# Kernel tuning notes

Measured on AMD Instinct MI355X. Metric: run time of the kernel, lower is better.

Reference implementation:

```python
import jax, jax.numpy as jnp
import numpy as np

N_CHANNELS = 1024
N_HEADS = 16
SEQ = 2048
BATCH = 2


def setup_inputs() -> dict:
    key = jax.random.key(0)
    k1, k2, k3 = jax.random.split(key, 3)
    x = jax.random.normal(k1, (BATCH, SEQ, N_CHANNELS), dtype=jnp.float32)
    qkv_w = jax.random.normal(k2, (3 * N_CHANNELS, N_CHANNELS), dtype=jnp.float32) * 0.02
    qkv_b = jnp.zeros((3 * N_CHANNELS,), dtype=jnp.float32)
    proj_w = jax.random.normal(k3, (N_CHANNELS, N_CHANNELS), dtype=jnp.float32) * 0.02
    proj_b = jnp.zeros((N_CHANNELS,), dtype=jnp.float32)
    return {"x": x, "qkv_w": qkv_w, "qkv_b": qkv_b, "proj_w": proj_w, "proj_b": proj_b}


def reference(x, qkv_w, qkv_b, proj_w, proj_b):
    bs, t, c = x.shape
    h = N_HEADS
    hd = c // h
    scale = hd ** (-0.5)
    # qkv projection: torch Linear is x @ W^T + b
    qkv = x @ qkv_w.T + qkv_b  # [B, T, 3C]
    qkv = qkv.reshape(bs, t, 3, h, hd)
    q, k, v = qkv[:, :, 0], qkv[:, :, 1], qkv[:, :, 2]  # each [B, T, H, hd]
    logits = jnp.einsum('bthc,bshc->bhts', q, k) * scale  # [B, H, T, T]
    # causal mask: log(tril(ones)) -> 0 below diag, -inf above
    causal = jnp.tril(jnp.ones((t, t), dtype=bool))
    logits = jnp.where(causal[None, None], logits, -jnp.inf)
    attn = jax.nn.softmax(logits, axis=-1)
    out = jnp.einsum('bhts,bshc->bthc', attn, v).reshape(bs, t, c)
    out = out @ proj_w.T + proj_b
    return out
```

## Files before the change

### kernel.cpp

```cpp
#include <hip/hip_runtime.h>

typedef __bf16 bf16x8 __attribute__((ext_vector_type(8)));
typedef float f32x4 __attribute__((ext_vector_type(4)));
typedef float f32x16 __attribute__((ext_vector_type(16)));

__device__ inline ushort f2bf(float f) {
    unsigned u = __builtin_bit_cast(unsigned, f);
    unsigned r = (u + 0x7FFFu + ((u >> 16) & 1u)) >> 16;
    return (ushort)r;
}
__device__ inline float bf2f(ushort u) {
    unsigned x = ((unsigned)u) << 16;
    return __builtin_bit_cast(float, x);
}
__device__ inline uint4 pack8(const float* f) {
    uint4 r;
    r.x = (unsigned)f2bf(f[0]) | ((unsigned)f2bf(f[1]) << 16);
    r.y = (unsigned)f2bf(f[2]) | ((unsigned)f2bf(f[3]) << 16);
    r.z = (unsigned)f2bf(f[4]) | ((unsigned)f2bf(f[5]) << 16);
    r.w = (unsigned)f2bf(f[6]) | ((unsigned)f2bf(f[7]) << 16);
    return r;
}
__device__ inline unsigned cvtpk_bf16(float lo, float hi) {
    unsigned r;
    asm("v_cvt_pk_bf16_f32 %0, %1, %2" : "=v"(r) : "v"(lo), "v"(hi));
    return r;
}

#define MFMA_BF16(a, b, c) __builtin_amdgcn_mfma_f32_16x16x32_bf16(a, b, c, 0, 0, 0)
#define MFMA32(a, b, c) __builtin_amdgcn_mfma_f32_32x32x16_bf16(a, b, c, 0, 0, 0)
#define GLDS(g, l) __builtin_amdgcn_global_load_lds( \
    (const __attribute__((address_space(1))) void*)(g), \
    (__attribute__((address_space(3))) void*)(l), 16, 0, 0)

#define QSCALE 0.18033688011112042f

__global__ __launch_bounds__(256) void convert3(
    const float* __restrict__ s0, ushort* __restrict__ d0,
    const float* __restrict__ s1, ushort* __restrict__ d1,
    const float* __restrict__ s2, ushort* __restrict__ d2)
{
    const int i = blockIdx.x * 256 + threadIdx.x;
    const float* s; ushort* d; int off;
    if (i < 524288)      { s = s0; d = d0; off = i; }
    else if (i < 917504) { s = s1; d = d1; off = i - 524288; }
    else                 { s = s2; d = d2; off = i - 917504; }
    const float4* f = (const float4*)s + off * 2;
    float fa[8];
    *(float4*)&fa[0] = f[0];
    *(float4*)&fa[4] = f[1];
    ((uint4*)d)[off] = pack8(fa);
}

__global__ __launch_bounds__(256) void gemm_qkv(
    const ushort* __restrict__ A, const ushort* __restrict__ B,
    const float* __restrict__ bias,
    ushort* __restrict__ outQ, ushort* __restrict__ outK, ushort* __restrict__ outV,
    int N, int K)
{
    __shared__ __align__(16) ushort SMEM[32768];

    const int tid = threadIdx.x;
    const int w = tid >> 6;
    const int lane = tid & 63;
    const int l15 = lane & 15;
    const int quad = lane >> 4;
    const int srow = lane >> 3;

    const int bid = blockIdx.x + (blockIdx.y << 5);
    const int nb = (bid & 7) * 96 + (bid >> 3);
    const int m0 = (nb / 24) * 128;
    const int n0 = (nb % 24) * 128;
    const int wr = (w & 1) * 64;
    const int wc = (w >> 1) * 64;

    auto stage = [&](int k0, int buf) {
        ushort* As = SMEM + buf * 16384;
        ushort* Bs = As + 8192;
#pragma unroll
        for (int j = 0; j < 4; j++) {
            const int r0 = w * 32 + j * 8;
            const int row = r0 + srow;
            const int gcol = ((lane & 7) ^ (row & 7)) * 8;
            GLDS(A + (size_t)(m0 + row) * K + k0 + gcol, As + r0 * 64);
            GLDS(B + (size_t)(n0 + row) * K + k0 + gcol, Bs + r0 * 64);
        }
    };

    f32x4 acc[4][4] = {};

    stage(0, 0);
    __syncthreads();

    for (int k0 = 0; k0 < K; k0 += 64) {
        const int cur = (k0 >> 6) & 1;
        if (k0 + 64 < K) stage(k0 + 64, cur ^ 1);

        const ushort* As = SMEM + cur * 16384;
        const ushort* Bs = As + 8192;
        bf16x8 af[4][2], bf[4][2];
#pragma unroll
        for (int i = 0; i < 4; i++)
#pragma unroll
            for (int kk = 0; kk < 2; kk++) {
                const int ra = wr + i * 16 + l15;
                const int rb = wc + i * 16 + l15;
                af[i][kk] = *(const bf16x8*)&As[ra * 64 + (((kk * 4 + quad) ^ (ra & 7)) * 8)];
                bf[i][kk] = *(const bf16x8*)&Bs[rb * 64 + (((kk * 4 + quad) ^ (rb & 7)) * 8)];
            }
#pragma unroll
        for (int kk = 0; kk < 2; kk++)
#pragma unroll
            for (int mi = 0; mi < 4; mi++)
#pragma unroll
                for (int ni = 0; ni < 4; ni++)
                    acc[mi][ni] = MFMA_BF16(af[mi][kk], bf[ni][kk], acc[mi][ni]);
        __syncthreads();
    }

    const int which = n0 >> 10;
    ushort* Ct = SMEM;
    if (which == 2) {
#pragma unroll
        for (int mi = 0; mi < 4; mi++)
#pragma unroll
            for (int ni = 0; ni < 4; ni++)
#pragma unroll
                for (int r = 0; r < 4; r++) {
                    const int m_loc = wr + mi * 16 + quad * 4 + r;
                    const int n_loc = wc + ni * 16 + l15;
                    Ct[n_loc * 136 + m_loc] =
                        f2bf(acc[mi][ni][r] + bias[n0 + n_loc]);
                }
        __syncthreads();
        const int b = m0 >> 11;
#pragma unroll
        for (int i = 0; i < 8; i++) {
            const int vi = tid + i * 256;
            const int n_loc = vi >> 4, mblk = vi & 15;
            const uint4 val = *(const uint4*)&Ct[n_loc * 136 + mblk * 8];
            const int t = (m0 & 2047) + mblk * 8;
            const int c = (n0 + n_loc) & 1023;
            const int h = c >> 6, d = c & 63;
            *(uint4*)&outV[((size_t)(b * 16 + h) * 64 + d) * 2048 + t] = val;
        }
    } else {
        const float qs = (which == 0) ? QSCALE : 1.0f;
#pragma unroll
        for (int mi = 0; mi < 4; mi++)
#pragma unroll
            for (int ni = 0; ni < 4; ni++)
#pragma unroll
                for (int r = 0; r < 4; r++) {
                    const int m_loc = wr + mi * 16 + quad * 4 + r;
                    const int n_loc = wc + ni * 16 + l15;
                    Ct[m_loc * 136 + n_loc] =
                        f2bf((acc[mi][ni][r] + bias[n0 + n_loc]) * qs);
                }
        __syncthreads();
        ushort* outP = (which == 0) ? outQ : outK;
        const int hb = (n0 & 1023) >> 6;
        const int b = m0 >> 11;
#pragma unroll
        for (int i = 0; i < 8; i++) {
            const int vi = tid + i * 256;
            const int m_loc = vi >> 4, u = vi & 15;
            const uint4 val = *(const uint4*)&Ct[m_loc * 136 + u * 8];
            const int t = (m0 & 2047) + m_loc;
            const int h = hb + (u >> 3);
            const int d8 = (u & 7) * 8;
            *(uint4*)&outP[((size_t)(b * 16 + h)) * 131072 + (size_t)t * 64 + d8] = val;
        }
    }
}

__global__ __launch_bounds__(256) void gemm_proj(
    const ushort* __restrict__ A, const ushort* __restrict__ B,
    const float* __restrict__ bias, float* __restrict__ outD)
{
    const int N = 1024, K = 1024;
    __shared__ __align__(16) ushort SMEM[24576];

    const int tid = threadIdx.x;
    const int w = tid >> 6;
    const int lane = tid & 63;
    const int l15 = lane & 15;
    const int quad = lane >> 4;
    const int srow = lane >> 3;

    const int bid = blockIdx.x + (blockIdx.y << 6);
    const int nb = (bid & 7) * 64 + (bid >> 3);
    const int m0 = (nb >> 3) * 64;
    const int n0 = (nb & 7) * 128;
    const int wr = (w & 1) * 32;
    const int wc = (w >> 1) * 64;

    auto stage = [&](int k0, int buf) {
        ushort* As = SMEM + buf * 12288;
        ushort* Bs = As + 4096;
#pragma unroll
        for (int j = 0; j < 2; j++) {
            const int r0 = w * 16 + j * 8;
            const int row = r0 + srow;
            const int gcol = ((lane & 7) ^ (row & 7)) * 8;
            GLDS(A + (size_t)(m0 + row) * K + k0 + gcol, As + r0 * 64);
        }
#pragma unroll
        for (int j = 0; j < 4; j++) {
            const int r0 = w * 32 + j * 8;
            const int row = r0 + srow;
            const int gcol = ((lane & 7) ^ (row & 7)) * 8;
            GLDS(B + (size_t)(n0 + row) * K + k0 + gcol, Bs + r0 * 64);
        }
    };

    f32x4 acc[2][4] = {};

    stage(0, 0);
    __syncthreads();

    for (int k0 = 0; k0 < K; k0 += 64) {
        const int cur = (k0 >> 6) & 1;
        if (k0 + 64 < K) stage(k0 + 64, cur ^ 1);

        const ushort* As = SMEM + cur * 12288;
        const ushort* Bs = As + 4096;
        bf16x8 af[2][2], bf[4][2];
#pragma unroll
        for (int kk = 0; kk < 2; kk++) {
#pragma unroll
            for (int mi = 0; mi < 2; mi++) {
                const int ra = wr + mi * 16 + l15;
                af[mi][kk] = *(const bf16x8*)&As[ra * 64 + (((kk * 4 + quad) ^ (ra & 7)) * 8)];
            }
#pragma unroll
            for (int ni = 0; ni < 4; ni++) {
                const int rb = wc + ni * 16 + l15;
                bf[ni][kk] = *(const bf16x8*)&Bs[rb * 64 + (((kk * 4 + quad) ^ (rb & 7)) * 8)];
            }
        }
#pragma unroll
        for (int kk = 0; kk < 2; kk++)
#pragma unroll
            for (int mi = 0; mi < 2; mi++)
#pragma unroll
                for (int ni = 0; ni < 4; ni++)
                    acc[mi][ni] = MFMA_BF16(af[mi][kk], bf[ni][kk], acc[mi][ni]);
        __syncthreads();
    }

    float* Cf = (float*)SMEM;
#pragma unroll
    for (int cch = 0; cch < 2; cch++) {
        __syncthreads();
        if ((wc >> 6) == cch) {
#pragma unroll
            for (int mi = 0; mi < 2; mi++)
#pragma unroll
                for (int ni = 0; ni < 4; ni++)
#pragma unroll
                    for (int r = 0; r < 4; r++) {
                        const int m_loc = wr + mi * 16 + quad * 4 + r;
                        const int nl = ni * 16 + l15;
                        Cf[m_loc * 68 + nl] = acc[mi][ni][r] + bias[n0 + cch * 64 + nl];
                    }
        }
        __syncthreads();
#pragma unroll
        for (int i = 0; i < 4; i++) {
            const int vi = tid + i * 256;
            const int m_loc = vi >> 4, u = vi & 15;
            const float4 val = *(const float4*)&Cf[m_loc * 68 + u * 4];
            *(float4*)&outD[(size_t)(m0 + m_loc) * N + n0 + cch * 64 + u * 4] = val;
        }
    }
}

__global__ __launch_bounds__(256, 4) void attn_split(
    const ushort* __restrict__ Q, const ushort* __restrict__ K,
    const ushort* __restrict__ Vt, ushort* __restrict__ O,
    ushort* __restrict__ Opart, float* __restrict__ Lpart)
{
    __shared__ __align__(16) ushort KV[2][2][64 * 64];

    const int bh = blockIdx.x;
    const int y = blockIdx.y;
    int qt, k0, k1, chunk, split;
    if (y < 24) {
        qt = 15 - (y >> 1); chunk = y & 1; split = 1;
        const int h2 = qt + 1;
        k0 = chunk ? h2 : 0; k1 = chunk ? 2 * qt + 2 : h2;
    } else {
        qt = 27 - y; chunk = 0; split = 0; k0 = 0; k1 = 2 * qt + 2;
    }
    const int q0 = qt * 128;
    const int tid = threadIdx.x;
    const int w = tid >> 6;
    const int lane = tid & 63;
    const int l31 = lane & 31;
    const int hf = lane >> 5;
    const int wrow0 = q0 + w * 32;
    const int rowg = wrow0 + l31;

    auto stage = [&](int kt, int b) {
        const int t0 = kt * 64;
#pragma unroll
        for (int j = 0; j < 2; j++) {
            const int r0 = w * 16 + j * 8;
            const int row = r0 + (lane >> 3);
            const int gcol = ((lane & 7) ^ (row & 7)) * 8;
            GLDS(K + ((size_t)bh * 2048 + t0 + row) * 64 + gcol, &KV[b][0][r0 * 64]);
            GLDS(Vt + ((size_t)bh * 64 + row) * 2048 + t0 + gcol, &KV[b][1][r0 * 64]);
        }
    };

    const ushort* qbase = Q + ((size_t)bh * 2048 + rowg) * 64 + hf * 8;
    bf16x8 qf[4];
#pragma unroll
    for (int db = 0; db < 4; db++) qf[db] = *(const bf16x8*)(qbase + db * 16);

    bf16x8 ones;
#pragma unroll
    for (int j = 0; j < 8; j++) ones[j] = (__bf16)1.0f;

    f32x16 oacc[2] = {};
    f32x16 lacc = {};

    stage(k0, 0);

    for (int kt = k0; kt < k1; kt++) {
        __syncthreads();
        if (kt + 1 < k1) stage(kt + 1, (kt + 1 - k0) & 1);

        const ushort* Ks = &KV[(kt - k0) & 1][0][0];
        const ushort* Vs = &KV[(kt - k0) & 1][1][0];
        const int t0 = kt * 64;

        if (t0 <= wrow0 + 31) {
            f32x16 sacc[2] = {};
#pragma unroll
            for (int db = 0; db < 4; db++)
#pragma unroll
                for (int kb = 0; kb < 2; kb++) {
                    const int rr = kb * 32 + l31;
                    bf16x8 kf = *(const bf16x8*)&Ks[rr * 64 + (((db * 2 + hf) ^ (rr & 7)) * 8)];
                    sacc[kb] = MFMA32(kf, qf[db], sacc[kb]);
                }

            unsigned u[2][8];
            const bool nm = (t0 + 63 > wrow0);
#pragma unroll
            for (int kb = 0; kb < 2; kb++) {
                float p[16];
                if (nm) {
#pragma unroll
                    for (int reg = 0; reg < 16; reg++) {
                        const int col = t0 + kb * 32 + (reg & 3) + 8 * (reg >> 2) + 4 * hf;
                        float x = (col > rowg) ? -1e30f : sacc[kb][reg];
                        p[reg] = __builtin_exp2f(x);
                    }
                } else {
#pragma unroll
                    for (int reg = 0; reg < 16; reg++)
                        p[reg] = __builtin_exp2f(sacc[kb][reg]);
                }
#pragma unroll
                for (int t = 0; t < 8; t++)
                    u[kb][t] = cvtpk_bf16(p[2 * t], p[2 * t + 1]);
            }

#pragma unroll
            for (int kb = 0; kb < 2; kb++)
#pragma unroll
                for (int g = 0; g < 4; g++) {
                    const int tp = (g & 1) + (g >> 1) * 4;
                    asm("v_permlane32_swap_b32 %0, %1"
                        : "+v"(u[kb][tp]), "+v"(u[kb][tp + 2]));
                }

#pragma unroll
            for (int m = 0; m < 4; m++) {
                uint4 av;
                av.x = u[m >> 1][(m & 1) * 4 + 0];
                av.y = u[m >> 1][(m & 1) * 4 + 1];
                av.z = u[m >> 1][(m & 1) * 4 + 2];
                av.w = u[m >> 1][(m & 1) * 4 + 3];
                bf16x8 af = __builtin_bit_cast(bf16x8, av);
                lacc = MFMA32(af, ones, lacc);
#pragma unroll
                for (int d2 = 0; d2 < 2; d2++) {
                    const int rr = d2 * 32 + l31;
                    bf16x8 vf = *(const bf16x8*)&Vs[rr * 64 + (((m * 2 + hf) ^ (rr & 7)) * 8)];
                    oacc[d2] = MFMA32(af, vf, oacc[d2]);
                }
            }
        }
    }

    if (!split) {
        const int b = bh >> 4, hh = bh & 15;
#pragma unroll
        for (int reg = 0; reg < 16; reg++) {
            const int rowf = (reg & 3) + 8 * (reg >> 2) + 4 * hf;
            const float inv = 1.0f / lacc[reg];
            const int row = wrow0 + rowf;
#pragma unroll
            for (int d2 = 0; d2 < 2; d2++)
                O[((size_t)b * 2048 + row) * 1024 + hh * 64 + d2 * 32 + l31] =
                    f2bf(oacc[d2][reg] * inv);
        }
    } else {
        const size_t slot2 = ((size_t)bh * 12 + (qt - 4)) * 2 + chunk;
        if (l31 == 0) {
#pragma unroll
            for (int reg = 0; reg < 16; reg++)
                Lpart[slot2 * 128 + w * 32 + (reg & 3) + 8 * (reg >> 2) + 4 * hf] = lacc[reg];
        }
#pragma unroll
        for (int reg = 0; reg < 16; reg++) {
            const int rl = w * 32 + (reg & 3) + 8 * (reg >> 2) + 4 * hf;
#pragma unroll
            for (int d2 = 0; d2 < 2; d2++)
                Opart[slot2 * 8192 + rl * 64 + d2 * 32 + l31] = f2bf(oacc[d2][reg]);
        }
    }
}

__global__ __launch_bounds__(256) void attn_combine(
    const ushort* __restrict__ Opart, const float* __restrict__ Lpart,
    ushort* __restrict__ O)
{
    const int bh = blockIdx.x;
    const int qt = 4 + blockIdx.y;
    const int tid = threadIdx.x;
    const int row = tid >> 1;
    const int dg = (tid & 1) * 32;
    const size_t s = ((size_t)bh * 12 + (qt - 4)) * 2;
    const ushort* p0 = Opart + s * 8192 + row * 64 + dg;
    const ushort* p1 = p0 + 8192;
    const float inv = 1.0f / (Lpart[s * 128 + row] + Lpart[(s + 1) * 128 + row]);
    const int b = bh >> 4, hh = bh & 15;
    ushort* dst = O + ((size_t)b * 2048 + qt * 128 + row) * 1024 + hh * 64 + dg;
#pragma unroll
    for (int v = 0; v < 4; v++) {
        uint4 a = *(const uint4*)(p0 + v * 8);
        uint4 c = *(const uint4*)(p1 + v * 8);
        const ushort* ua = (const ushort*)&a;
        const ushort* uc = (const ushort*)&c;
        ushort out[8];
#pragma unroll
        for (int j = 0; j < 8; j++)
            out[j] = f2bf((bf2f(ua[j]) + bf2f(uc[j])) * inv);
        *(uint4*)(dst + v * 8) = *(uint4*)out;
    }
}

extern "C" void kernel_launch(void* const* d_in, const int* in_sizes, int n_in,
                              void* d_out, int out_size, void* d_ws, size_t ws_size,
                              hipStream_t stream) {
    const float* x      = (const float*)d_in[0];
    const float* qkv_w  = (const float*)d_in[1];
    const float* qkv_b  = (const float*)d_in[2];
    const float* proj_w = (const float*)d_in[3];
    const float* proj_b = (const float*)d_in[4];

    ushort* XbOb  = (ushort*)d_ws + 16;
    ushort* Wqkv  = XbOb + 4194304;
    ushort* Wproj = Wqkv + 3145728;
    ushort* Qb    = Wproj + 1048576;
    ushort* Kb    = Qb + 4194304;
    ushort* Vt    = Kb + 4194304;
    ushort* Opart = Vt + 4194304;
    float*  Lpart = (float*)(Opart + 6291456);

    convert3<<<4096, 256, 0, stream>>>(x, XbOb, qkv_w, Wqkv, proj_w, Wproj);
    gemm_qkv<<<dim3(32, 24), 256, 0, stream>>>(XbOb, Wqkv, qkv_b,
                                               Qb, Kb, Vt, 3072, 1024);
    attn_split<<<dim3(32, 28), 256, 0, stream>>>(Qb, Kb, Vt, XbOb, Opart, Lpart);
    attn_combine<<<dim3(32, 12), 256, 0, stream>>>(Opart, Lpart, XbOb);
    gemm_proj<<<dim3(64, 8), 256, 0, stream>>>(XbOb, Wproj, proj_b, (float*)d_out);
}
```

Baseline: 209.1 us.

## Rebalance causal attention split with 2/3/4-way KV chunks and staged coalesced output

Longer causal query tiles are now split into 2, 3 or 4 KV chunks according to their length instead of always 2, raising the grid from 28 to 40 tiles per head so per-block work is more even. Block IDs are remapped so that neighbouring IDs land on different XCDs, output tiles are staged through shared memory for coalesced 16-byte stores, and the occupancy hint rises to 5. The combine kernel now sums a variable number of partials, and the Opart buffer reuses the Wqkv workspace region. The cost is more partial-result traffic and combine work, plus an added barrier in each block.

```diff
diff --git a/kernel.cpp b/kernel.cpp
--- a/kernel.cpp
+++ b/kernel.cpp
@@ -276,22 +276,32 @@
     }
 }
 
-__global__ __launch_bounds__(256, 4) void attn_split(
+__global__ __launch_bounds__(256, 5) void attn_split(
     const ushort* __restrict__ Q, const ushort* __restrict__ K,
     const ushort* __restrict__ Vt, ushort* __restrict__ O,
     ushort* __restrict__ Opart, float* __restrict__ Lpart)
 {
     __shared__ __align__(16) ushort KV[2][2][64 * 64];
 
-    const int bh = blockIdx.x;
-    const int y = blockIdx.y;
-    int qt, k0, k1, chunk, split;
-    if (y < 24) {
-        qt = 15 - (y >> 1); chunk = y & 1; split = 1;
-        const int h2 = qt + 1;
-        k0 = chunk ? h2 : 0; k1 = chunk ? 2 * qt + 2 : h2;
+    const int bid0 = blockIdx.x + blockIdx.y * 32;
+    const int nb = (bid0 & 7) * 160 + (bid0 >> 3);
+    const int bh = (nb / 160) * 4 + (nb % 160) / 40;
+    const int y = nb % 40;
+
+    int qt, k0, k1, split;
+    const int slot = y - 4;
+    if (y < 4) {
+        qt = y; k0 = 0; k1 = 2 * qt + 2; split = 0;
     } else {
-        qt = 27 - y; chunk = 0; split = 0; k0 = 0; k1 = 2 * qt + 2;
+        split = 1;
+        const int z = y - 4;
+        int ci, c;
+        if (z < 8)       { qt = 4 + (z >> 1); ci = z & 1; c = 2; }
+        else if (z < 20) { const int t = z - 8;  qt = 8 + t / 3;   ci = t % 3; c = 3; }
+        else             { const int t = z - 20; qt = 12 + (t >> 2); ci = t & 3; c = 4; }
+        const int n = 2 * qt + 2;
+        k0 = ci * n / c;
+        k1 = (ci + 1) * n / c;
     }
     const int q0 = qt * 128;
     const int tid = threadIdx.x;
@@ -397,21 +407,10 @@
         }
     }
 
-    if (!split) {
-        const int b = bh >> 4, hh = bh & 15;
-#pragma unroll
-        for (int reg = 0; reg < 16; reg++) {
-            const int rowf = (reg & 3) + 8 * (reg >> 2) + 4 * hf;
-            const float inv = 1.0f / lacc[reg];
-            const int row = wrow0 + rowf;
-#pragma unroll
-            for (int d2 = 0; d2 < 2; d2++)
-                O[((size_t)b * 2048 + row) * 1024 + hh * 64 + d2 * 32 + l31] =
-                    f2bf(oacc[d2][reg] * inv);
-        }
-    } else {
-        const size_t slot2 = ((size_t)bh * 12 + (qt - 4)) * 2 + chunk;
+    ushort* Ob = &KV[(k1 - k0) & 1][0][0];
+    if (split) {
         if (l31 == 0) {
+            const size_t slot2 = (size_t)bh * 36 + slot;
 #pragma unroll
             for (int reg = 0; reg < 16; reg++)
                 Lpart[slot2 * 128 + w * 32 + (reg & 3) + 8 * (reg >> 2) + 4 * hf] = lacc[reg];
@@ -421,7 +420,35 @@
             const int rl = w * 32 + (reg & 3) + 8 * (reg >> 2) + 4 * hf;
 #pragma unroll
             for (int d2 = 0; d2 < 2; d2++)
-                Opart[slot2 * 8192 + rl * 64 + d2 * 32 + l31] = f2bf(oacc[d2][reg]);
+                Ob[rl * 64 + d2 * 32 + l31] = f2bf(oacc[d2][reg]);
+        }
+    } else {
+#pragma unroll
+        for (int reg = 0; reg < 16; reg++) {
+            const float inv = 1.0f / lacc[reg];
+            const int rl = w * 32 + (reg & 3) + 8 * (reg >> 2) + 4 * hf;
+#pragma unroll
+            for (int d2 = 0; d2 < 2; d2++)
+                Ob[rl * 64 + d2 * 32 + l31] = f2bf(oacc[d2][reg] * inv);
+        }
+    }
+    __syncthreads();
+    if (split) {
+        const size_t slot2 = (size_t)bh * 36 + slot;
+        ushort* dst = Opart + slot2 * 8192;
+#pragma unroll
+        for (int i = 0; i < 4; i++) {
+            const int idx = tid + i * 256;
+            *(uint4*)&dst[idx * 8] = *(const uint4*)&Ob[idx * 8];
+        }
+    } else {
+        const int b = bh >> 4, hh = bh & 15;
+#pragma unroll
+        for (int i = 0; i < 4; i++) {
+            const int idx = tid + i * 256;
+            const int rl = idx >> 3, c0 = (idx & 7) * 8;
+            *(uint4*)&O[((size_t)b * 2048 + q0 + rl) * 1024 + hh * 64 + c0] =
+                *(const uint4*)&Ob[idx * 8];
         }
     }
 }
@@ -432,25 +459,32 @@
 {
     const int bh = blockIdx.x;
     const int qt = 4 + blockIdx.y;
+    const int c = (qt >> 2) + 1;
+    int base;
+    if (qt < 8)       base = (qt - 4) * 2;
+    else if (qt < 12) base = 8 + (qt - 8) * 3;
+    else              base = 20 + (qt - 12) * 4;
     const int tid = threadIdx.x;
     const int row = tid >> 1;
     const int dg = (tid & 1) * 32;
-    const size_t s = ((size_t)bh * 12 + (qt - 4)) * 2;
-    const ushort* p0 = Opart + s * 8192 + row * 64 + dg;
-    const ushort* p1 = p0 + 8192;
-    const float inv = 1.0f / (Lpart[s * 128 + row] + Lpart[(s + 1) * 128 + row]);
+    const size_t s = (size_t)bh * 36 + base;
+    float lsum = 0.f;
+    for (int j = 0; j < c; j++) lsum += Lpart[(s + j) * 128 + row];
+    const float inv = 1.0f / lsum;
     const int b = bh >> 4, hh = bh & 15;
     ushort* dst = O + ((size_t)b * 2048 + qt * 128 + row) * 1024 + hh * 64 + dg;
 #pragma unroll
     for (int v = 0; v < 4; v++) {
-        uint4 a = *(const uint4*)(p0 + v * 8);
-        uint4 c = *(const uint4*)(p1 + v * 8);
-        const ushort* ua = (const ushort*)&a;
-        const ushort* uc = (const ushort*)&c;
+        float accf[8] = {};
+        for (int j = 0; j < c; j++) {
+            uint4 a = *(const uint4*)(Opart + (s + j) * 8192 + row * 64 + dg + v * 8);
+            const ushort* ua = (const ushort*)&a;
+#pragma unroll
+            for (int t = 0; t < 8; t++) accf[t] += bf2f(ua[t]);
+        }
         ushort out[8];
 #pragma unroll
-        for (int j = 0; j < 8; j++)
-            out[j] = f2bf((bf2f(ua[j]) + bf2f(uc[j])) * inv);
+        for (int t = 0; t < 8; t++) out[t] = f2bf(accf[t] * inv);
         *(uint4*)(dst + v * 8) = *(uint4*)out;
     }
 }
@@ -465,18 +499,18 @@
     const float* proj_b = (const float*)d_in[4];
 
     ushort* XbOb  = (ushort*)d_ws + 16;
-    ushort* Wqkv  = XbOb + 4194304;
-    ushort* Wproj = Wqkv + 3145728;
+    ushort* Wproj = XbOb + 4194304;
     ushort* Qb    = Wproj + 1048576;
     ushort* Kb    = Qb + 4194304;
     ushort* Vt    = Kb + 4194304;
-    ushort* Opart = Vt + 4194304;
-    float*  Lpart = (float*)(Opart + 6291456);
+    ushort* Wqkv  = Vt + 4194304;
+    ushort* Opart = Wqkv;
+    float*  Lpart = (float*)(Opart + 9437184);
 
     convert3<<<4096, 256, 0, stream>>>(x, XbOb, qkv_w, Wqkv, proj_w, Wproj);
     gemm_qkv<<<dim3(32, 24), 256, 0, stream>>>(XbOb, Wqkv, qkv_b,
                                                Qb, Kb, Vt, 3072, 1024);
-    attn_split<<<dim3(32, 28), 256, 0, stream>>>(Qb, Kb, Vt, XbOb, Opart, Lpart);
+    attn_split<<<dim3(32, 40), 256, 0, stream>>>(Qb, Kb, Vt, XbOb, Opart, Lpart);
     attn_combine<<<dim3(32, 12), 256, 0, stream>>>(Opart, Lpart, XbOb);
     gemm_proj<<<dim3(64, 8), 256, 0, stream>>>(XbOb, Wproj, proj_b, (float*)d_out);
 }
```

Result: slower. 298.6 us (+42.8%).
